# Optimization experiments

Hardware: AMD Instinct MI355X
Metric: run time of the kernel (lower is better)

The kernel has to match this reference:

```python
import jax, jax.numpy as jnp
import numpy as np

H, W = 4096, 4096
KH, KW = 11, 11


def setup_inputs() -> dict:
    key = jax.random.key(0)
    k1, k2 = jax.random.split(key)
    x = jax.random.normal(k1, (H, W), dtype=jnp.float32)
    weight = jax.random.uniform(k2, (KH, KW), dtype=jnp.float32)
    bias = jnp.zeros((1,), dtype=jnp.float32)
    return {"x": x, "weight": weight, "bias": bias}


def reference(x, weight, bias):
    # corr2d: valid 2D cross-correlation of a single-channel image with a
    # single kernel, then add scalar bias. Output shape [H-KH+1, W-KW+1].
    out = jax.lax.conv_general_dilated(
        x[None, None, :, :],            # NCHW, N=C=1
        weight[None, None, :, :],       # OIHW, O=I=1
        window_strides=(1, 1),
        padding="VALID",
        dimension_numbers=("NCHW", "OIHW", "NCHW"),
    )[0, 0]
    return out + bias[0]
```

## Files before the change

### kernel.cpp

```cpp
#include <hip/hip_runtime.h>
#include <hip/hip_bf16.h>

#define IH 4096
#define IW 4096
#define KH 11
#define KW 11
#define OH (IH - KH + 1)
#define OW (IW - KW + 1)

#define BM 64
#define BN 64
#define TROWS   74
#define TSTRIDE 84
#define NC4     20
#define NCHUNK  (TROWS * NC4)
#define NITER   6
#define TILE_SHORTS (TROWS * TSTRIDE)

#define TILES_X 64
#define NBLK    1024

typedef short bf16x4 __attribute__((ext_vector_type(4)));
typedef short bf16x8 __attribute__((ext_vector_type(8)));
typedef float f32x4  __attribute__((ext_vector_type(4)));

__device__ __forceinline__ short f2b(float f) {
    __hip_bfloat16 h = __float2bfloat16(f);
    return __builtin_bit_cast(short, h);
}

__device__ __forceinline__ void stage_load(float4 G[NITER],
                                           const float* __restrict__ x,
                                           int gx0, int gy0, int tid) {
#pragma unroll
    for (int it = 0; it < NITER; ++it) {
        const int i = tid + it * 256;
        float4 v = make_float4(0.f, 0.f, 0.f, 0.f);
        if (i < NCHUNK) {
            const int r  = i / NC4;
            const int c4 = i - r * NC4;
            const int gy = gy0 + r;
            const int gx = gx0 + c4 * 4;
            if (gy < IH && gx + 3 < IW) {
                v = *reinterpret_cast<const float4*>(x + (size_t)gy * IW + gx);
            }
        }
        G[it] = v;
    }
}

__device__ __forceinline__ void stage_write(short* __restrict__ tb,
                                            const float4 G[NITER], int tid) {
#pragma unroll
    for (int it = 0; it < NITER; ++it) {
        const int i = tid + it * 256;
        if (i < NCHUNK) {
            const int r  = i / NC4;
            const int c4 = i - r * NC4;
            bf16x4 b = { f2b(G[it].x), f2b(G[it].y), f2b(G[it].z), f2b(G[it].w) };
            *reinterpret_cast<bf16x4*>(&tb[r * TSTRIDE + c4 * 4]) = b;
        }
    }
}

__device__ __forceinline__ void compute_tile(const short* __restrict__ tb,
                                             const short* __restrict__ bmat,
                                             float bv, float* __restrict__ out,
                                             int gx0, int gy0,
                                             int wv, int g, int li) {
    f32x4 acc[4] = {};
    const short* ap = &tb[(16 * wv + li) * TSTRIDE + g * 8];
    const short* bp = &bmat[li * 32 + g * 8];

#pragma unroll 1
    for (int kh = 0; kh < KH; ++kh) {
        const bf16x8 bfrag = *reinterpret_cast<const bf16x8*>(bp + kh * 512);
#pragma unroll
        for (int c = 0; c < 4; ++c) {
            bf16x4 lo = *reinterpret_cast<const bf16x4*>(ap + c * 16);
            bf16x4 hi = *reinterpret_cast<const bf16x4*>(ap + c * 16 + 4);
            bf16x8 a  = __builtin_shufflevector(lo, hi, 0, 1, 2, 3, 4, 5, 6, 7);
            acc[c] = __builtin_amdgcn_mfma_f32_16x16x32_bf16(a, bfrag, acc[c],
                                                             0, 0, 0);
        }
        ap += TSTRIDE;
    }

#pragma unroll
    for (int c = 0; c < 4; ++c) {
        const int ox = gx0 + c * 16 + li;
        if (ox < OW) {
#pragma unroll
            for (int r = 0; r < 4; ++r) {
                const int oy = gy0 + wv * 16 + g * 4 + r;
                if (oy < OH) {
                    out[(size_t)oy * OW + ox] = acc[c][r] + bv;
                }
            }
        }
    }
}

__global__ __launch_bounds__(256)
void conv2d_mfma4(const float* __restrict__ x,
                  const float* __restrict__ w,
                  const float* __restrict__ bias,
                  float* __restrict__ out) {
    __shared__ short buf[2][TILE_SHORTS];
    __shared__ short bmat[KH * 512];

    const int tid = threadIdx.x;
    const int blk = (blockIdx.x & 7) * (NBLK / 8) + (blockIdx.x >> 3);
    const int t0  = blk * 4;
    const int gy0 = (t0 >> 6) * BM;
    const int gxb = (t0 & (TILES_X - 1)) * BN;

    const int lane = tid & 63;
    const int wv   = tid >> 6;
    const int g    = lane >> 4;
    const int li   = lane & 15;
    const float bv = bias[0];

    {
        float4 G0[NITER];
        stage_load(G0, x, gxb, gy0, tid);
        stage_write(buf[0], G0, tid);
    }
#pragma unroll
    for (int t = 0; t < 22; ++t) {
        const int idx = tid + t * 256;
        const int kh = idx >> 9;
        const int j  = (idx >> 5) & 15;
        const int k  = idx & 31;
        const int d  = k - j;
        const float val = (d >= 0 && d < KW) ? w[kh * KW + d] : 0.f;
        bmat[idx] = f2b(val);
    }
    __syncthreads();

    float4 G[NITER];
#pragma unroll 1
    for (int t = 0; t < 4; ++t) {
        if (t < 3) {
            stage_load(G, x, gxb + (t + 1) * BN, gy0, tid);
            __builtin_amdgcn_sched_barrier(0);
        }
        compute_tile(buf[t & 1], bmat, bv, out, gxb + t * BN, gy0, wv, g, li);
        if (t < 3) {
            stage_write(buf[(t + 1) & 1], G, tid);
            __syncthreads();
        }
    }
}

extern "C" void kernel_launch(void* const* d_in, const int* in_sizes, int n_in,
                              void* d_out, int out_size, void* d_ws, size_t ws_size,
                              hipStream_t stream) {
    const float* x    = (const float*)d_in[0];
    const float* w    = (const float*)d_in[1];
    const float* bias = (const float*)d_in[2];
    float* out        = (float*)d_out;

    dim3 grid(NBLK);
    dim3 block(256);
    conv2d_mfma4<<<grid, block, 0, stream>>>(x, w, bias, out);
}
```

Measured before the change: 40.94 us.

## Reuse A fragments across kernel rows via DPP row shifts instead of LDS reloads

The input fragments stay in registers. For each kernel row, each lane takes the next image row from its neighbour lane using a DPP row_shr:1 (0x101), so only one new row per 16-lane group is fetched from LDS instead of every lane reloading its row. LDS reads become single 16-byte loads (stride padded from 84 to 88 shorts for alignment), and the B fragment is prefetched one step ahead. This cuts LDS traffic in the MFMA inner loop but adds DPP instructions, more registers, and tricky lane-boundary correctness.

```diff
diff --git a/kernel.cpp b/kernel.cpp
--- a/kernel.cpp
+++ b/kernel.cpp
@@ -11,7 +11,7 @@
 #define BM 64
 #define BN 64
 #define TROWS   74
-#define TSTRIDE 84
+#define TSTRIDE 88
 #define NC4     20
 #define NCHUNK  (TROWS * NC4)
 #define NITER   6
@@ -23,6 +23,7 @@
 typedef short bf16x4 __attribute__((ext_vector_type(4)));
 typedef short bf16x8 __attribute__((ext_vector_type(8)));
 typedef float f32x4  __attribute__((ext_vector_type(4)));
+typedef int   i32x4  __attribute__((ext_vector_type(4)));
 
 __device__ __forceinline__ short f2b(float f) {
     __hip_bfloat16 h = __float2bfloat16(f);
@@ -63,28 +64,54 @@
     }
 }
 
+__device__ __forceinline__ void mfma4(f32x4 acc[4], const i32x4 F[4], bf16x8 b) {
+#pragma unroll
+    for (int c = 0; c < 4; ++c) {
+        acc[c] = __builtin_amdgcn_mfma_f32_16x16x32_bf16(
+            __builtin_bit_cast(bf16x8, F[c]), b, acc[c], 0, 0, 0);
+    }
+}
+
 __device__ __forceinline__ void compute_tile(const short* __restrict__ tb,
                                              const short* __restrict__ bmat,
                                              float bv, float* __restrict__ out,
                                              int gx0, int gy0,
                                              int wv, int g, int li) {
     f32x4 acc[4] = {};
-    const short* ap = &tb[(16 * wv + li) * TSTRIDE + g * 8];
-    const short* bp = &bmat[li * 32 + g * 8];
+    const short* abase = &tb[(16 * wv + li) * TSTRIDE + g * 8];
+    const short* fbase = &tb[(16 * wv) * TSTRIDE + g * 8];
+    const short* bp    = &bmat[li * 32 + g * 8];
+
+    i32x4 F[4], FR[4];
+#pragma unroll
+    for (int c = 0; c < 4; ++c)
+        F[c] = *reinterpret_cast<const i32x4*>(abase + c * 16);
+    bf16x8 Bcur = *reinterpret_cast<const bf16x8*>(bp);
+#pragma unroll
+    for (int c = 0; c < 4; ++c)
+        FR[c] = *reinterpret_cast<const i32x4*>(fbase + 16 * TSTRIDE + c * 16);
+    bf16x8 Bnext = *reinterpret_cast<const bf16x8*>(bp + 512);
 
 #pragma unroll 1
-    for (int kh = 0; kh < KH; ++kh) {
-        const bf16x8 bfrag = *reinterpret_cast<const bf16x8*>(bp + kh * 512);
+    for (int kh = 0; kh < KH - 1; ++kh) {
+        mfma4(acc, F, Bcur);
 #pragma unroll
         for (int c = 0; c < 4; ++c) {
-            bf16x4 lo = *reinterpret_cast<const bf16x4*>(ap + c * 16);
-            bf16x4 hi = *reinterpret_cast<const bf16x4*>(ap + c * 16 + 4);
-            bf16x8 a  = __builtin_shufflevector(lo, hi, 0, 1, 2, 3, 4, 5, 6, 7);
-            acc[c] = __builtin_amdgcn_mfma_f32_16x16x32_bf16(a, bfrag, acc[c],
-                                                             0, 0, 0);
+#pragma unroll
+            for (int d = 0; d < 4; ++d) {
+                F[c][d] = __builtin_amdgcn_update_dpp(
+                    FR[c][d], F[c][d], 0x101 , 0xF, 0xF, false);
+            }
         }
-        ap += TSTRIDE;
+        const int nr = (kh + 17 > 25) ? 25 : kh + 17;
+#pragma unroll
+        for (int c = 0; c < 4; ++c)
+            FR[c] = *reinterpret_cast<const i32x4*>(fbase + nr * TSTRIDE + c * 16);
+        Bcur = Bnext;
+        const int nb = (kh + 2 > 10) ? 10 : kh + 2;
+        Bnext = *reinterpret_cast<const bf16x8*>(bp + nb * 512);
     }
+    mfma4(acc, F, Bcur);
 
 #pragma unroll
     for (int c = 0; c < 4; ++c) {
@@ -102,10 +129,10 @@
 }
 
 __global__ __launch_bounds__(256)
-void conv2d_mfma4(const float* __restrict__ x,
-                  const float* __restrict__ w,
-                  const float* __restrict__ bias,
-                  float* __restrict__ out) {
+void conv2d_dpp(const float* __restrict__ x,
+                const float* __restrict__ w,
+                const float* __restrict__ bias,
+                float* __restrict__ out) {
     __shared__ short buf[2][TILE_SHORTS];
     __shared__ short bmat[KH * 512];
 
@@ -163,5 +190,5 @@
 
     dim3 grid(NBLK);
     dim3 block(256);
-    conv2d_mfma4<<<grid, block, 0, stream>>>(x, w, bias, out);
+    conv2d_dpp<<<grid, block, 0, stream>>>(x, w, bias, out);
 }
```

Measured after the change: 51.05 us. 24.7% more time.
